# Kernel tuning notes

Hardware: AMD Instinct MI355X
Metric: run time of the kernel (lower is better)

The kernel has to match this reference:

```python
import jax, jax.numpy as jnp
import numpy as np

B, N, K, UP = 8, 2048, 20, 2
CIN, D, COUT, PH, AH = 256, 64, 128, 64, 256
EPS = 1e-5

def c1(x, W, b):
    # 1x1 Conv1d: x (B,C,N), W (O,C)
    return jnp.einsum('oc,bcn->bon', W, x) + b[None, :, None]

def c2(x, W, b):
    # 1x1 Conv2d: x (B,C,N,K), W (O,C)
    return jnp.einsum('oc,bcnk->bonk', W, x) + b[None, :, None, None]

def bn2(x, g, be):
    # eval-mode BatchNorm2d with running_mean=0, running_var=1
    inv = np.float32(1.0 / np.sqrt(1.0 + EPS))
    return g[None, :, None, None] * x * inv + be[None, :, None, None]

def knn_idx(p, k):
    # p: (B,N,3) -> (B,N,k) indices of k nearest neighbors (incl. self)
    sq = jnp.sum(p * p, -1)
    d = sq[:, :, None] + sq[:, None, :] - 2.0 * jnp.einsum('bnd,bmd->bnm', p, p)
    _, idx = jax.lax.top_k(-d, k)
    return idx

def group(feat, idx):
    # grouping_operation: feat (B,C,N), idx (B,N,k) -> (B,C,N,k)
    return jax.vmap(lambda f, i: f[:, i])(feat, idx)

def setup_inputs() -> dict:
    key = jax.random.key(0)
    ks = jax.random.split(key, 24)
    s = 0.02
    rn = lambda i, shp: jax.random.normal(ks[i], shp, jnp.float32) * s
    return {
        'pos': jax.random.normal(ks[0], (B, 3, N), jnp.float32),
        'key_feat': jax.random.normal(ks[1], (B, CIN, N), jnp.float32),
        'query_feat': jax.random.normal(ks[2], (B, CIN, N), jnp.float32),
        'upfeat': jax.random.normal(ks[3], (B, CIN, N), jnp.float32),
        # mlp_v (MLP_Res): in 2*CIN -> CIN -> CIN with shortcut
        'Wv1': rn(4, (CIN, 2 * CIN)), 'bv1': jnp.zeros(CIN, jnp.float32),
        'Wv2': rn(5, (CIN, CIN)), 'bv2': jnp.zeros(CIN, jnp.float32),
        'Wvs': rn(6, (CIN, 2 * CIN)), 'bvs': jnp.zeros(CIN, jnp.float32),
        # key/query/value/upfeat 1x1 convs CIN -> D
        'Wk': rn(7, (D, CIN)), 'bk': jnp.zeros(D, jnp.float32),
        'Wq': rn(8, (D, CIN)), 'bq': jnp.zeros(D, jnp.float32),
        'Wvv': rn(9, (D, CIN)), 'bvv': jnp.zeros(D, jnp.float32),
        'Wu': rn(10, (D, CIN)), 'bu': jnp.zeros(D, jnp.float32),
        # pos_mlp: 3 -> PH (BN, ReLU) -> D
        'Wp1': rn(11, (PH, 3)), 'bp1': jnp.zeros(PH, jnp.float32),
        'gp1': jnp.ones(PH, jnp.float32), 'betap1': jnp.zeros(PH, jnp.float32),
        'Wp2': rn(12, (D, PH)), 'bp2': jnp.zeros(D, jnp.float32),
        # attn_mlp: D -> AH (BN, ReLU) -> ConvTranspose2d(AH, D, (UP,1), (UP,1))
        'Wa1': rn(13, (AH, D)), 'ba1': jnp.zeros(AH, jnp.float32),
        'ga1': jnp.ones(AH, jnp.float32), 'betaa1': jnp.zeros(AH, jnp.float32),
        'Wt': rn(14, (AH, D, UP)), 'bt': jnp.zeros(D, jnp.float32),
        # conv_end D -> COUT, residual CIN -> COUT
        'Wend': rn(15, (COUT, D)), 'bend': jnp.zeros(COUT, jnp.float32),
        'Wres': rn(16, (COUT, CIN)), 'bres': jnp.zeros(COUT, jnp.float32),
    }

def reference(pos, key_feat, query_feat, upfeat,
              Wv1, bv1, Wv2, bv2, Wvs, bvs,
              Wk, bk, Wq, bq, Wvv, bvv, Wu, bu,
              Wp1, bp1, gp1, betap1, Wp2, bp2,
              Wa1, ba1, ga1, betaa1, Wt, bt,
              Wend, bend, Wres, bres):
    # mlp_v on concat(key, query)
    x = jnp.concatenate([key_feat, query_feat], axis=1)          # (B,2CIN,N)
    value = c1(jax.nn.relu(c1(x, Wv1, bv1)), Wv2, bv2) + c1(x, Wvs, bvs)
    identity = value                                             # (B,CIN,N)
    kf = c1(key_feat, Wk, bk)
    qf = c1(query_feat, Wq, bq)
    vf = c1(value, Wvv, bvv)                                     # (B,D,N)
    idx = knn_idx(pos.transpose(0, 2, 1), K)                     # (B,N,K)
    kg = group(kf, idx)                                          # (B,D,N,K)
    qk_rel = qf[:, :, :, None] - kg
    pos_rel = pos[:, :, :, None] - group(pos, idx)               # (B,3,N,K)
    pos_emb = c2(jax.nn.relu(bn2(c2(pos_rel, Wp1, bp1), gp1, betap1)), Wp2, bp2)
    uf = c1(upfeat, Wu, bu)
    u_rel = uf[:, :, :, None] - group(uf, idx)                   # (B,D,N,K)
    h = jax.nn.relu(bn2(c2(qk_rel + pos_emb + u_rel, Wa1, ba1), ga1, betaa1))  # (B,AH,N,K)
    b = h.shape[0]
    # ConvTranspose2d kernel (UP,1) stride (UP,1): expand N -> N*UP
    att = jnp.einsum('bhnk,hcr->bcnrk', h, Wt).reshape(b, D, N * UP, K) + bt[None, :, None, None]
    att = jax.nn.softmax(att, axis=-1)
    val = group(vf, idx) + pos_emb + u_rel                       # (B,D,N,K)
    val = jnp.repeat(val, UP, axis=2)                            # nearest Upsample (UP,1)
    agg = jnp.sum(att * val, axis=-1)                            # (B,D,N*UP)
    y = c1(agg, Wend, bend)                                      # (B,COUT,N*UP)
    ident = jnp.repeat(c1(identity, Wres, bres), UP, axis=2)     # residual path
    return y + ident
```

## Files before the change

kernel.cpp:

```cpp
#include <hip/hip_runtime.h>
#include <hip/hip_bf16.h>
#include <math.h>

#define BB 8
#define NN 2048
#define KK 20
#define UPF 2
#define CIN 256
#define DD 64
#define COUTN 128
#define PHH 64
#define AHH 256
#define BN_INV 0.9999950000374997f
#define NPB 8

typedef __hip_bfloat16 bf16;
typedef unsigned short u16;
typedef unsigned long long u64;
typedef _Float16 f16;
typedef _Float16 h2   __attribute__((ext_vector_type(2)));
typedef _Float16 f16x4 __attribute__((ext_vector_type(4)));
typedef _Float16 f16x8 __attribute__((ext_vector_type(8)));
typedef float    f32x4 __attribute__((ext_vector_type(4)));

static __device__ __forceinline__ float bf2f(const bf16 v) { return __bfloat162float(v); }
static __device__ __forceinline__ bf16  f2bf(const float v) { return __float2bfloat16(v); }
static __device__ __forceinline__ u16   f2bfu(const float v) {
    return __builtin_bit_cast(u16, __float2bfloat16(v));
}
static __device__ __forceinline__ float lo2f(const unsigned v) { return __builtin_bit_cast(float, v << 16); }
static __device__ __forceinline__ float hi2f(const unsigned v) { return __builtin_bit_cast(float, v & 0xFFFF0000u); }

static __device__ __forceinline__ f32x4 mfma16(const f16x8 a, const f16x8 b, const f32x4 c) {
    return __builtin_amdgcn_mfma_f32_16x16x32_f16(a, b, c, 0, 0, 0);
}
static __device__ __forceinline__ unsigned fmap(const float f) {
    unsigned u = __builtin_bit_cast(unsigned, f);
    return (u >> 31) ? ~u : (u | 0x80000000u);
}

__global__ void sentinel_kernel(float* out) {
    if (threadIdx.x == 0 && blockIdx.x == 0) out[0] = 100.0f;
}

__global__ __launch_bounds__(256) void prep_kernel(
    const float* __restrict__ Wa1, const float* __restrict__ Wp2,
    const float* __restrict__ Wend, const float* __restrict__ Wt,
    const float* __restrict__ Wv1, const float* __restrict__ Wv2,
    const float* __restrict__ Wvs, const float* __restrict__ Wvv,
    const float* __restrict__ Wres,
    const float* __restrict__ Wk, const float* __restrict__ Wq,
    const float* __restrict__ Wu,
    const float* __restrict__ ba1, const float* __restrict__ ga1,
    const float* __restrict__ betaa1,
    f16* __restrict__ Wa1h, f16* __restrict__ Wp2h, f16* __restrict__ Wth,
    float* __restrict__ A1s, float* __restrict__ A1b,
    f16* __restrict__ Wendh,
    f16* __restrict__ Wv1h, f16* __restrict__ Wv2h, f16* __restrict__ Wvsh,
    f16* __restrict__ Wvvh, f16* __restrict__ Wresh,
    f16* __restrict__ Wkh, f16* __restrict__ Wqh, f16* __restrict__ Wuh) {
    const int t = blockIdx.x * 256 + threadIdx.x;
    if (t < AHH * DD)        Wa1h[t] = (f16)Wa1[t];
    if (t < PHH * DD)        Wp2h[t] = (f16)Wp2[t];
    if (t < COUTN * AHH)     { int cr = t >> 8, hh = t & 255; Wth[t] = (f16)Wt[hh * COUTN + cr]; }
    if (t < AHH) {
        float gsc = ga1[t] * BN_INV;
        A1s[t] = gsc;
        A1b[t] = gsc * ba1[t] + betaa1[t];
    }
    if (t < COUTN * DD)      Wendh[t] = (f16)Wend[t];
    if (t < CIN * 2 * CIN)   Wv1h[t] = (f16)Wv1[t];
    if (t < CIN * CIN)       Wv2h[t] = (f16)Wv2[t];
    if (t < CIN * 2 * CIN)   Wvsh[t] = (f16)Wvs[t];
    if (t < DD * CIN)        Wvvh[t] = (f16)Wvv[t];
    if (t < COUTN * CIN)     Wresh[t] = (f16)Wres[t];
    if (t < DD * CIN)        Wkh[t]  = (f16)Wk[t];
    if (t < DD * CIN)        Wqh[t]  = (f16)Wq[t];
    if (t < DD * CIN)        Wuh[t]  = (f16)Wu[t];
}

__global__ __launch_bounds__(256) void xpose_kernel(
    const float* __restrict__ key_feat, const float* __restrict__ query_feat,
    const float* __restrict__ upfeat,
    f16* __restrict__ xkqT, f16* __restrict__ xuT) {
    __shared__ float tile[64][65];
    const int b  = blockIdx.x >> 5;
    const int n0 = (blockIdx.x & 31) << 6;
    const int y  = blockIdx.y;
    const int src = y >> 2;
    const int ct  = (y & 3) << 6;
    const int t = threadIdx.x;
    const float* xin = (src == 0) ? key_feat : (src == 1) ? query_feat : upfeat;
    f16* dst; int CT, cb;
    if (src < 2) { dst = xkqT; CT = 512; cb = src * 256 + ct; }
    else         { dst = xuT;  CT = 256; cb = ct; }
    for (int u = t; u < 64 * 64; u += 256) {
        const int c = u >> 6, j = u & 63;
        tile[c][j] = xin[((size_t)b * CIN + ct + c) * NN + n0 + j];
    }
    __syncthreads();
    for (int u = t; u < 64 * 32; u += 256) {
        const int n = u >> 5, c0 = (u & 31) << 1;
        h2 pr; pr.x = (f16)tile[c0][n]; pr.y = (f16)tile[c0 + 1][n];
        ((unsigned*)dst)[(((size_t)b * NN + n0 + n) * CT + cb + c0) >> 1] =
            __builtin_bit_cast(unsigned, pr);
    }
}

__global__ __launch_bounds__(256) void knn_kernel(const float* __restrict__ pos,
                                                  u16* __restrict__ idx_out,
                                                  float* __restrict__ posT) {
    __shared__ float dist[NN];
    __shared__ int   hist[512];
    __shared__ unsigned rmin[4], rmax[4];
    __shared__ u64   cbuf[64];
    __shared__ float q[3];
    __shared__ unsigned minkS;
    __shared__ int   shiftS, jstarS, cntS;
    __shared__ u64   ltbuf[KK];
    __shared__ int   tiebuf[64];
    __shared__ int   ri[4];
    __shared__ unsigned prefS;
    __shared__ int   knS, cnt_lt, cnt_eq;

    const int b = blockIdx.x / NN;
    const int n = blockIdx.x % NN;
    const int t = threadIdx.x;
    const float* pb = pos + (size_t)b * 3 * NN;
    const size_t rowKK = ((size_t)b * NN + n) * KK;

    if (t < 3) {
        float v = pb[(size_t)t * NN + n];
        q[t] = v;
        posT[((size_t)b * NN + n) * 3 + t] = v;
    }
    if (t == 0) { prefS = 0u; knS = KK; cnt_lt = 0; cnt_eq = 0; cntS = 0; jstarS = 0; }
    __syncthreads();
    const float qx = q[0], qy = q[1], qz = q[2];
    const float sqq = __fadd_rn(__fadd_rn(__fmul_rn(qx, qx), __fmul_rn(qy, qy)), __fmul_rn(qz, qz));
    unsigned kmin = 0xFFFFFFFFu, kmax = 0u;
    for (int m = t; m < NN; m += 256) {
        float px = pb[m];
        float py = pb[NN + m];
        float pz = pb[2 * NN + m];
        float sqm = __fadd_rn(__fadd_rn(__fmul_rn(px, px), __fmul_rn(py, py)), __fmul_rn(pz, pz));
        float dt  = __fadd_rn(__fadd_rn(__fmul_rn(qx, px), __fmul_rn(qy, py)), __fmul_rn(qz, pz));
        const float d = __fsub_rn(__fadd_rn(sqq, sqm), __fmul_rn(2.0f, dt));
        dist[m] = d;
        const unsigned key = fmap(d);
        kmin = min(kmin, key);
        kmax = max(kmax, key);
    }
#pragma unroll
    for (int off = 32; off > 0; off >>= 1) {
        kmin = min(kmin, (unsigned)__shfl_down((int)kmin, off, 64));
        kmax = max(kmax, (unsigned)__shfl_down((int)kmax, off, 64));
    }
    if ((t & 63) == 0) { rmin[t >> 6] = kmin; rmax[t >> 6] = kmax; }
    hist[t] = 0; hist[256 + t] = 0;
    __syncthreads();
    if (t == 0) {
        const unsigned mn = min(min(rmin[0], rmin[1]), min(rmin[2], rmin[3]));
        const unsigned mx = max(max(rmax[0], rmax[1]), max(rmax[2], rmax[3]));
        const unsigned range = mx - mn;
        minkS  = mn;
        shiftS = (range >= 256u) ? (24 - __clz((int)range)) : 0;
    }
    __syncthreads();
    const unsigned mink = minkS;
    const int sh = shiftS;

    for (int m = t; m < NN; m += 256) {
        const unsigned bin = (fmap(dist[m]) - mink) >> sh;
        atomicAdd(&hist[((unsigned)(t & 1) << 8) | bin], 1);
    }
    __syncthreads();
    if (t < 64) {
        const int h0  = hist[4 * t + 0] + hist[256 + 4 * t + 0];
        const int h1  = hist[4 * t + 1] + hist[256 + 4 * t + 1];
        const int h2v = hist[4 * t + 2] + hist[256 + 4 * t + 2];
        const int h3  = hist[4 * t + 3] + hist[256 + 4 * t + 3];
        const int lsum = h0 + h1 + h2v + h3;
        int incl = lsum;
#pragma unroll
        for (int off = 1; off < 64; off <<= 1) {
            int v = __shfl_up(incl, off, 64);
            if (t >= off) incl += v;
        }
        const int excl = incl - lsum;
        if (excl < KK && excl + lsum >= KK) {
            int bsel;
            if      (excl + h0 >= KK)            bsel = 0;
            else if (excl + h0 + h1 >= KK)       bsel = 1;
            else if (excl + h0 + h1 + h2v >= KK) bsel = 2;
            else                                 bsel = 3;
            jstarS = 4 * t + bsel;
        }
    }
    __syncthreads();
    const unsigned jstar = (unsigned)jstarS;

    for (int m = t; m < NN; m += 256) {
        const unsigned key = fmap(dist[m]);
        if (((key - mink) >> sh) <= jstar) {
            const int p = atomicAdd(&cntS, 1);
            if (p < 64) cbuf[p] = ((u64)key << 32) | (unsigned)m;
        }
    }
    __syncthreads();
    const int total = cntS;

    if (total <= 64) {
        if (t < 64) {
            u64 v = (t < total) ? cbuf[t] : 0xFFFFFFFFFFFFFFFFull;
            int rank = 0;
#pragma unroll 16
            for (int j = 0; j < 64; ++j) {
                const u64 o = (u64)__shfl((long long)v, j, 64);
                if (o < v) ++rank;
            }
            if (t < total && rank < KK) idx_out[rowKK + rank] = (u16)(v & 0xFFFFu);
        }
        return;
    }

    for (int pass = 0; pass < 4; ++pass) {
        const int shift = 24 - 8 * pass;
        const unsigned pm = (pass == 0) ? 0u : (0xFFFFFFFFu << (32 - 8 * pass));
        hist[t] = 0;
        __syncthreads();
        const unsigned pref = prefS;
        const int kn = knS;
        for (int m = t; m < NN; m += 256) {
            unsigned key = fmap(dist[m]);
            if ((key & pm) == pref)
                atomicAdd(&hist[(key >> shift) & 255], 1);
        }
        __syncthreads();
        if (t < 64) {
            const int h0 = hist[4 * t + 0], h1 = hist[4 * t + 1];
            const int h2v = hist[4 * t + 2], h3 = hist[4 * t + 3];
            const int lsum = h0 + h1 + h2v + h3;
            int incl = lsum;
#pragma unroll
            for (int off = 1; off < 64; off <<= 1) {
                int v = __shfl_up(incl, off, 64);
                if (t >= off) incl += v;
            }
            const int excl = incl - lsum;
            if (excl < kn && excl + lsum >= kn) {
                int bsel, cb;
                if      (excl + h0 >= kn)            { bsel = 0; cb = excl; }
                else if (excl + h0 + h1 >= kn)       { bsel = 1; cb = excl + h0; }
                else if (excl + h0 + h1 + h2v >= kn) { bsel = 2; cb = excl + h0 + h1; }
                else                                 { bsel = 3; cb = excl + h0 + h1 + h2v; }
                knS = kn - cb;
                prefS = pref | ((unsigned)(4 * t + bsel) << shift);
            }
        }
        __syncthreads();
    }

    const unsigned T = prefS;
    for (int m = t; m < NN; m += 256) {
        unsigned key = fmap(dist[m]);
        if (key < T) {
            int p = atomicAdd(&cnt_lt, 1);
            ltbuf[p] = ((u64)key << 32) | (unsigned)m;
        } else if (key == T) {
            int p = atomicAdd(&cnt_eq, 1);
            if (p < 64) tiebuf[p] = m;
        }
    }
    __syncthreads();
    const int nlt = cnt_lt, neq_need = knS, ceq = cnt_eq;

    if (t < 64) {
        u64 v = (t < nlt) ? ltbuf[t] : 0xFFFFFFFFFFFFFFFFull;
        int rank = 0;
#pragma unroll
        for (int j = 0; j < KK; ++j) {
            const u64 o = (u64)__shfl((long long)v, j, 64);
            if (o < v) ++rank;
        }
        if (t < nlt) idx_out[rowKK + rank] = (u16)(v & 0xFFFFu);
    }
    if (ceq <= 64) {
        if (t < 64) {
            int ti = (t < ceq) ? tiebuf[t] : 0x7FFFFFFF;
            int rk = 0;
            for (int j = 0; j < 64; ++j) {
                const int o = __shfl(ti, j, 64);
                if (o < ti) ++rk;
            }
            if (t < ceq && rk < neq_need) idx_out[rowKK + nlt + rk] = (u16)ti;
        }
    } else {
        for (int iter = 0; iter < neq_need; ++iter) {
            int bi = NN;
            for (int m = t; m < NN; m += 256)
                if (fmap(dist[m]) == T && m < bi) bi = m;
            for (int off = 32; off > 0; off >>= 1) {
                int i2 = __shfl_down(bi, off, 64);
                bi = min(bi, i2);
            }
            if ((t & 63) == 0) ri[t >> 6] = bi;
            __syncthreads();
            if (t == 0) {
                int i0 = min(min(ri[0], ri[1]), min(ri[2], ri[3]));
                idx_out[rowKK + nlt + iter] = (u16)i0;
                dist[i0] = 3.4e38f;
            }
            __syncthreads();
        }
    }
}

__global__ __launch_bounds__(256) void value_mfma(
    const f16* __restrict__ xkqT, const f16* __restrict__ xuT,
    const f16* __restrict__ Wv1h, const float* __restrict__ bv1,
    const f16* __restrict__ Wv2h, const float* __restrict__ bv2,
    const f16* __restrict__ Wvsh, const float* __restrict__ bvs,
    const f16* __restrict__ Wvvh, const float* __restrict__ bvv,
    const f16* __restrict__ Wresh, const float* __restrict__ bres,
    const f16* __restrict__ Wkh, const float* __restrict__ bk,
    const f16* __restrict__ Wqh, const float* __restrict__ bq,
    const f16* __restrict__ Wuh, const float* __restrict__ bu,
    bf16* __restrict__ vf_ws, bf16* __restrict__ resid_ws,
    bf16* __restrict__ kf, bf16* __restrict__ qf, bf16* __restrict__ uf) {
    __shared__ __align__(16) char hv[32 * 512];
    const int b  = blockIdx.x >> 6;
    const int n0 = (blockIdx.x & 63) << 5;
    const int t = threadIdx.x;
    const int w = t >> 6, l = t & 63, g = l >> 4, li = l & 15;
    const f16* xb = xkqT + ((size_t)b * NN + n0) * 512;
    const f32x4 zero4 = {0.f, 0.f, 0.f, 0.f};

    f32x4 a1[4][2];
    f32x4 ak[2] = {zero4, zero4}, aq[2] = {zero4, zero4};
#pragma unroll
    for (int mt = 0; mt < 4; ++mt) { a1[mt][0] = zero4; a1[mt][1] = zero4; }
    for (int ks = 0; ks < 16; ++ks) {
        f16x8 bx0 = *(const f16x8*)(xb + (size_t)li * 512 + ks * 32 + g * 8);
        f16x8 bx1 = *(const f16x8*)(xb + (size_t)(16 + li) * 512 + ks * 32 + g * 8);
#pragma unroll
        for (int mt = 0; mt < 4; ++mt) {
            const f16x8 af = *(const f16x8*)(Wv1h + (size_t)(w * 64 + mt * 16 + li) * 512 + ks * 32 + g * 8);
            a1[mt][0] = mfma16(af, bx0, a1[mt][0]);
            a1[mt][1] = mfma16(af, bx1, a1[mt][1]);
        }
        if (ks < 8) {
            const f16x8 afk = *(const f16x8*)(Wkh + (size_t)(w * 16 + li) * 256 + ks * 32 + g * 8);
            ak[0] = mfma16(afk, bx0, ak[0]);
            ak[1] = mfma16(afk, bx1, ak[1]);
        } else {
            const f16x8 afq = *(const f16x8*)(Wqh + (size_t)(w * 16 + li) * 256 + (ks - 8) * 32 + g * 8);
            aq[0] = mfma16(afq, bx0, aq[0]);
            aq[1] = mfma16(afq, bx1, aq[1]);
        }
    }
    f32x4 au[2] = {zero4, zero4};
    {
        const f16* xub = xuT + ((size_t)b * NN + n0) * 256;
        for (int ks = 0; ks < 8; ++ks) {
            f16x8 bu0 = *(const f16x8*)(xub + (size_t)li * 256 + ks * 32 + g * 8);
            f16x8 bu1 = *(const f16x8*)(xub + (size_t)(16 + li) * 256 + ks * 32 + g * 8);
            const f16x8 af = *(const f16x8*)(Wuh + (size_t)(w * 16 + li) * 256 + ks * 32 + g * 8);
            au[0] = mfma16(af, bu0, au[0]);
            au[1] = mfma16(af, bu1, au[1]);
        }
    }
#pragma unroll
    for (int mt = 0; mt < 4; ++mt) {
        const int ch0 = w * 64 + mt * 16 + g * 4;
        const float4 b4 = *(const float4*)(bv1 + ch0);
#pragma unroll
        for (int nt = 0; nt < 2; ++nt) {
            const int n = nt * 16 + li;
            f16x4 px;
            px.x = (f16)fmaxf(a1[mt][nt][0] + b4.x, 0.f);
            px.y = (f16)fmaxf(a1[mt][nt][1] + b4.y, 0.f);
            px.z = (f16)fmaxf(a1[mt][nt][2] + b4.z, 0.f);
            px.w = (f16)fmaxf(a1[mt][nt][3] + b4.w, 0.f);
            *(f16x4*)(hv + n * 512 + ((ch0 * 2) ^ ((n & 7) << 4))) = px;
        }
    }
    {
        const int ch0 = w * 16 + g * 4;
        const float4 bk4 = *(const float4*)(bk + ch0);
        const float4 bq4 = *(const float4*)(bq + ch0);
        const float4 bu4 = *(const float4*)(bu + ch0);
#pragma unroll
        for (int nt = 0; nt < 2; ++nt) {
            const int n = nt * 16 + li;
            const size_t base = ((size_t)b * NN + n0 + n) * DD + ch0;
            ushort4 pk, pq, pu;
            pk.x = f2bfu(ak[nt][0] + bk4.x); pk.y = f2bfu(ak[nt][1] + bk4.y);
            pk.z = f2bfu(ak[nt][2] + bk4.z); pk.w = f2bfu(ak[nt][3] + bk4.w);
            pq.x = f2bfu(aq[nt][0] + bq4.x); pq.y = f2bfu(aq[nt][1] + bq4.y);
            pq.z = f2bfu(aq[nt][2] + bq4.z); pq.w = f2bfu(aq[nt][3] + bq4.w);
            pu.x = f2bfu(au[nt][0] + bu4.x); pu.y = f2bfu(au[nt][1] + bu4.y);
            pu.z = f2bfu(au[nt][2] + bu4.z); pu.w = f2bfu(au[nt][3] + bu4.w);
            *(ushort4*)((char*)kf + base * 2) = pk;
            *(ushort4*)((char*)qf + base * 2) = pq;
            *(ushort4*)((char*)uf + base * 2) = pu;
        }
    }
    __syncthreads();

    f32x4 a2[4][2];
#pragma unroll
    for (int mt = 0; mt < 4; ++mt) { a2[mt][0] = zero4; a2[mt][1] = zero4; }
    for (int ks = 0; ks < 8; ++ks) {
        f16x8 bh[2];
#pragma unroll
        for (int nt = 0; nt < 2; ++nt) {
            const int n = nt * 16 + li;
            bh[nt] = *(const f16x8*)(hv + n * 512 + ((ks * 64 + g * 16) ^ ((n & 7) << 4)));
        }
#pragma unroll
        for (int mt = 0; mt < 4; ++mt) {
            const f16x8 af = *(const f16x8*)(Wv2h + (size_t)(w * 64 + mt * 16 + li) * 256 + ks * 32 + g * 8);
            a2[mt][0] = mfma16(af, bh[0], a2[mt][0]);
            a2[mt][1] = mfma16(af, bh[1], a2[mt][1]);
        }
    }
    for (int ks = 0; ks < 16; ++ks) {
        f16x8 bx0 = *(const f16x8*)(xb + (size_t)li * 512 + ks * 32 + g * 8);
        f16x8 bx1 = *(const f16x8*)(xb + (size_t)(16 + li) * 512 + ks * 32 + g * 8);
#pragma unroll
        for (int mt = 0; mt < 4; ++mt) {
            const f16x8 af = *(const f16x8*)(Wvsh + (size_t)(w * 64 + mt * 16 + li) * 512 + ks * 32 + g * 8);
            a2[mt][0] = mfma16(af, bx0, a2[mt][0]);
            a2[mt][1] = mfma16(af, bx1, a2[mt][1]);
        }
    }
    __syncthreads();
#pragma unroll
    for (int mt = 0; mt < 4; ++mt) {
        const int ch0 = w * 64 + mt * 16 + g * 4;
        const float4 c4a = *(const float4*)(bv2 + ch0);
        const float4 c4b = *(const float4*)(bvs + ch0);
#pragma unroll
        for (int nt = 0; nt < 2; ++nt) {
            const int n = nt * 16 + li;
            f16x4 px;
            px.x = (f16)(a2[mt][nt][0] + c4a.x + c4b.x);
            px.y = (f16)(a2[mt][nt][1] + c4a.y + c4b.y);
            px.z = (f16)(a2[mt][nt][2] + c4a.z + c4b.z);
            px.w = (f16)(a2[mt][nt][3] + c4a.w + c4b.w);
            *(f16x4*)(hv + n * 512 + ((ch0 * 2) ^ ((n & 7) << 4))) = px;
        }
    }
    __syncthreads();

    f32x4 av[2] = {zero4, zero4};
    f32x4 ar[2][2];
    ar[0][0] = zero4; ar[0][1] = zero4; ar[1][0] = zero4; ar[1][1] = zero4;
    for (int ks = 0; ks < 8; ++ks) {
        f16x8 bh[2];
#pragma unroll
        for (int nt = 0; nt < 2; ++nt) {
            const int n = nt * 16 + li;
            bh[nt] = *(const f16x8*)(hv + n * 512 + ((ks * 64 + g * 16) ^ ((n & 7) << 4)));
        }
        const f16x8 afv = *(const f16x8*)(Wvvh + (size_t)(w * 16 + li) * 256 + ks * 32 + g * 8);
        av[0] = mfma16(afv, bh[0], av[0]);
        av[1] = mfma16(afv, bh[1], av[1]);
#pragma unroll
        for (int rt = 0; rt < 2; ++rt) {
            const f16x8 afr = *(const f16x8*)(Wresh + (size_t)((w * 2 + rt) * 16 + li) * 256 + ks * 32 + g * 8);
            ar[rt][0] = mfma16(afr, bh[0], ar[rt][0]);
            ar[rt][1] = mfma16(afr, bh[1], ar[rt][1]);
        }
    }
    {
        const int ch0 = w * 16 + g * 4;
        const float4 bb = *(const float4*)(bvv + ch0);
#pragma unroll
        for (int nt = 0; nt < 2; ++nt) {
            const int n = nt * 16 + li;
            ushort4 pk;
            pk.x = f2bfu(av[nt][0] + bb.x);
            pk.y = f2bfu(av[nt][1] + bb.y);
            pk.z = f2bfu(av[nt][2] + bb.z);
            pk.w = f2bfu(av[nt][3] + bb.w);
            *(ushort4*)((char*)vf_ws + (((size_t)b * NN + n0 + n) * DD + ch0) * 2) = pk;
        }
    }
#pragma unroll
    for (int rt = 0; rt < 2; ++rt) {
        const int ch0 = (w * 2 + rt) * 16 + g * 4;
        const float4 bb = *(const float4*)(bres + ch0);
#pragma unroll
        for (int nt = 0; nt < 2; ++nt) {
            const int n = nt * 16 + li;
            ushort4 pk;
            pk.x = f2bfu(ar[rt][nt][0] + bb.x);
            pk.y = f2bfu(ar[rt][nt][1] + bb.y);
            pk.z = f2bfu(ar[rt][nt][2] + bb.z);
            pk.w = f2bfu(ar[rt][nt][3] + bb.w);
            *(ushort4*)((char*)resid_ws + (((size_t)b * NN + n0 + n) * COUTN + ch0) * 2) = pk;
        }
    }
}

__global__ __launch_bounds__(512, 4) void attn_fused(
    const float* __restrict__ posT, const u16* __restrict__ idx_ws,
    const bf16* __restrict__ kf_ws, const bf16* __restrict__ qf_ws,
    const bf16* __restrict__ uf_ws, const bf16* __restrict__ vf_ws,
    const bf16* __restrict__ resid_ws,
    const float* __restrict__ Wp1, const float* __restrict__ bp1,
    const float* __restrict__ gp1, const float* __restrict__ betap1,
    const f16* __restrict__ Wp2h, const float* __restrict__ bp2,
    const f16* __restrict__ Wa1h, const float* __restrict__ A1s,
    const float* __restrict__ A1b, const f16* __restrict__ Wth,
    const f16* __restrict__ Wendh, const float* __restrict__ bend,
    float* __restrict__ out) {
    __shared__ __align__(16) char pool[61440];
    f16*  ph16 = (f16*)(pool);
    f16*  S16  = (f16*)(pool);
    f16*  L16T = (f16*)(pool);
    f16*  peh  = (f16*)(pool + 20480);
    char* Hl   = pool + 20480;
    f16*  V16  = (f16*)(pool + 40960);
    __shared__ __align__(16) f16 aggf[16 * 64];
    __shared__ int   nidx[8 * KK];
    __shared__ float prel[8 * KK][3];
    __shared__ float qcol[NPB][64], ucol[NPB][64];

    const int b  = blockIdx.x >> 8;
    const int n0 = (blockIdx.x & 255) << 3;
    const int t = threadIdx.x;
    const int w = t >> 6, l = t & 63, g = l >> 4, li = l & 15;
    const int m4 = w & 3, nh = w >> 2;
    const size_t row0 = (size_t)b * NN + n0;
    const f32x4 zero4 = {0.f, 0.f, 0.f, 0.f};

    if (t < 8 * KK) nidx[t] = (int)idx_ws[row0 * KK + t];
    __syncthreads();

    {
        const int n = t >> 6, c = t & 63;
        qcol[n][c] = bf2f(qf_ws[(row0 + n) * DD + c]);
        ucol[n][c] = bf2f(uf_ws[(row0 + n) * DD + c]);
    }
    if (t < 480) {
        const int r = t / 3, d = t - r * 3;
        const int n = r / KK;
        prel[r][d] = posT[(row0 + n) * 3 + d] - posT[((size_t)b * NN + nidx[r]) * 3 + d];
    }
    __syncthreads();

    for (int u = t; u < 160 * 32; u += 512) {
        const int r = u >> 5, c0 = (u & 31) << 1;
        float a0 = Wp1[c0 * 3 + 0] * prel[r][0] + Wp1[c0 * 3 + 1] * prel[r][1]
                 + Wp1[c0 * 3 + 2] * prel[r][2] + bp1[c0];
        float a1 = Wp1[c0 * 3 + 3] * prel[r][0] + Wp1[c0 * 3 + 4] * prel[r][1]
                 + Wp1[c0 * 3 + 5] * prel[r][2] + bp1[c0 + 1];
        a0 = gp1[c0] * a0 * BN_INV + betap1[c0];
        a1 = gp1[c0 + 1] * a1 * BN_INV + betap1[c0 + 1];
        h2 pr; pr.x = (f16)fmaxf(a0, 0.f); pr.y = (f16)fmaxf(a1, 0.f);
        *(unsigned*)((char*)ph16 + (r * 128 + ((c0 * 2) ^ ((r & 7) << 4)))) =
            __builtin_bit_cast(unsigned, pr);
    }
    __syncthreads();

    {
        f32x4 d[5];
#pragma unroll
        for (int j = 0; j < 5; ++j) d[j] = zero4;
#pragma unroll
        for (int ks = 0; ks < 2; ++ks) {
            const f16x8 af = *(const f16x8*)(Wp2h + (m4 * 16 + li) * 64 + ks * 32 + g * 8);
#pragma unroll
            for (int j = 0; j < 5; ++j) {
                const int r = (nh * 5 + j) * 16 + li;
                const f16x8 bf = *(const f16x8*)((const char*)ph16 +
                                  (r * 128 + ((ks * 64 + g * 16) ^ ((r & 7) << 4))));
                d[j] = mfma16(af, bf, d[j]);
            }
        }
        const int ch0 = m4 * 16 + g * 4;
        const float4 b4 = *(const float4*)(bp2 + ch0);
#pragma unroll
        for (int j = 0; j < 5; ++j) {
            const int r = (nh * 5 + j) * 16 + li;
            f16x4 pk;
            pk.x = (f16)(d[j][0] + b4.x);
            pk.y = (f16)(d[j][1] + b4.y);
            pk.z = (f16)(d[j][2] + b4.z);
            pk.w = (f16)(d[j][3] + b4.w);
            *(f16x4*)((char*)peh + (r * 128 + ((ch0 * 2) ^ ((r & 7) << 4)))) = pk;
        }
    }
    __syncthreads();

    for (int u = t; u < 160 * 32; u += 512) {
        const int r = u >> 5, c0 = (u & 31) << 1;
        const int n = r / KK;
        const size_t nb2 = (((size_t)b * NN + nidx[r]) * DD + c0) * 2;
        const unsigned kq = *(const unsigned*)((const char*)kf_ws + nb2);
        const unsigned uq = *(const unsigned*)((const char*)uf_ws + nb2);
        const unsigned vq = *(const unsigned*)((const char*)vf_ws + nb2);
        const unsigned pw = *(const unsigned*)((const char*)peh +
                              (r * 128 + ((c0 * 2) ^ ((r & 7) << 4))));
        const h2 pp = __builtin_bit_cast(h2, pw);
        const float add0 = ucol[n][c0] + (float)pp.x;
        const float add1 = ucol[n][c0 + 1] + (float)pp.y;
        const float gb0 = -(lo2f(kq) + lo2f(uq));
        const float gb1 = -(hi2f(kq) + hi2f(uq));
        const float vb0 = lo2f(vq) - lo2f(uq);
        const float vb1 = hi2f(vq) - hi2f(uq);
        h2 s; s.x = (f16)(gb0 + qcol[n][c0] + add0); s.y = (f16)(gb1 + qcol[n][c0 + 1] + add1);
        h2 v; v.x = (f16)(vb0 + add0);               v.y = (f16)(vb1 + add1);
        const int sw = (c0 * 2) ^ ((r & 7) << 4);
        *(unsigned*)((char*)S16 + (r * 128 + sw)) = __builtin_bit_cast(unsigned, s);
        *(unsigned*)((char*)V16 + (r * 128 + sw)) = __builtin_bit_cast(unsigned, v);
    }
    __syncthreads();

    f32x4 acc2[10];
#pragma unroll
    for (int j = 0; j < 10; ++j) acc2[j] = zero4;

    for (int c4 = 0; c4 < 4; ++c4) {
        const int hrb = c4 * 64 + m4 * 16;
        f32x4 d1[5];
#pragma unroll
        for (int j = 0; j < 5; ++j) d1[j] = zero4;
#pragma unroll
        for (int ks = 0; ks < 2; ++ks) {
            const f16x8 af = *(const f16x8*)(Wa1h + (hrb + li) * 64 + ks * 32 + g * 8);
#pragma unroll
            for (int j = 0; j < 5; ++j) {
                const int r = (nh * 5 + j) * 16 + li;
                const f16x8 sfv = *(const f16x8*)((const char*)S16 +
                                   (r * 128 + ((ks * 64 + g * 16) ^ ((r & 7) << 4))));
                d1[j] = mfma16(af, sfv, d1[j]);
            }
        }
        const float4 as4 = *(const float4*)(A1s + hrb + g * 4);
        const float4 ab4 = *(const float4*)(A1b + hrb + g * 4);
        __syncthreads();
#pragma unroll
        for (int j = 0; j < 5; ++j) {
            const int col = (nh * 5 + j) * 16 + li;
            const int ch0 = m4 * 16 + g * 4;
            f16x4 pk;
            pk.x = (f16)fmaxf(as4.x * d1[j][0] + ab4.x, 0.f);
            pk.y = (f16)fmaxf(as4.y * d1[j][1] + ab4.y, 0.f);
            pk.z = (f16)fmaxf(as4.z * d1[j][2] + ab4.z, 0.f);
            pk.w = (f16)fmaxf(as4.w * d1[j][3] + ab4.w, 0.f);
            *(f16x4*)(Hl + col * 128 + ((ch0 * 2) ^ ((col & 7) << 4))) = pk;
        }
        __syncthreads();
#pragma unroll
        for (int ks2 = 0; ks2 < 2; ++ks2) {
            const f16x8 bf = *(const f16x8*)(Wth + (size_t)(w * 16 + li) * AHH + c4 * 64 + ks2 * 32 + g * 8);
#pragma unroll
            for (int nt = 0; nt < 10; ++nt) {
                const int col = nt * 16 + li;
                const f16x8 ha = *(const f16x8*)(Hl + col * 128 + ((ks2 * 64 + g * 16) ^ ((col & 7) << 4)));
                acc2[nt] = mfma16(ha, bf, acc2[nt]);
            }
        }
    }
    __syncthreads();

#pragma unroll
    for (int nt = 0; nt < 10; ++nt) {
        const f32x4 d = acc2[nt];
#pragma unroll
        for (int j = 0; j < 4; ++j) {
            const int row = nt * 16 + g * 4 + j;
            *(f16*)((char*)L16T + (row * 256 + (((w * 16 + li) * 2) ^ ((row & 3) << 5)))) =
                (f16)d[j];
        }
    }
    __syncthreads();

    {
        const int cr = t & 127, c = cr >> 1, rr = cr & 1;
        const int nbase = (t >> 7) * 2;
        for (int p = 0; p < 2; ++p) {
            const int n = nbase + p;
            float lv[20];
#pragma unroll
            for (int k = 0; k < 20; ++k) {
                const int row = n * KK + k;
                lv[k] = (float)*(const f16*)((const char*)L16T +
                          (row * 256 + ((cr * 2) ^ ((row & 3) << 5))));
            }
            float m = lv[0];
#pragma unroll
            for (int k = 1; k < 20; ++k) m = fmaxf(m, lv[k]);
            float s = 0.f, a = 0.f;
#pragma unroll
            for (int k = 0; k < 20; ++k) {
                const float e = __expf(lv[k] - m);
                s += e;
                const int r = n * KK + k;
                const float vv = (float)*(const f16*)((const char*)V16 +
                                   (r * 128 + ((c * 2) ^ ((r & 7) << 4))));
                a += e * vv;
            }
            const int arow = n * 2 + rr;
            *(f16*)((char*)aggf + (arow * 128 + ((c * 2) ^ ((arow & 7) << 4)))) = (f16)(a / s);
        }
    }
    __syncthreads();

    {
        f32x4 dc = zero4;
#pragma unroll
        for (int ks = 0; ks < 2; ++ks) {
            const f16x8 af = *(const f16x8*)(Wendh + (size_t)(w * 16 + li) * 64 + ks * 32 + g * 8);
            const f16x8 bfr = *(const f16x8*)((const char*)aggf +
                               (li * 128 + (((ks * 32 + g * 8) * 2) ^ ((li & 7) << 4))));
            dc = mfma16(af, bfr, dc);
        }
        const int nloc = li >> 1;
#pragma unroll
        for (int j = 0; j < 4; ++j) {
            const int o = w * 16 + g * 4 + j;
            const float rv = bf2f(resid_ws[(row0 + nloc) * COUTN + o]);
            out[(size_t)b * COUTN * (NN * UPF) + (size_t)o * (NN * UPF) + 2 * n0 + li] =
                dc[j] + bend[o] + rv;
        }
    }
}

extern "C" void kernel_launch(void* const* d_in, const int* in_sizes, int n_in,
                              void* d_out, int out_size, void* d_ws, size_t ws_size,
                              hipStream_t stream) {
    const float* pos        = (const float*)d_in[0];
    const float* key_feat   = (const float*)d_in[1];
    const float* query_feat = (const float*)d_in[2];
    const float* upfeat     = (const float*)d_in[3];
    const float* Wv1 = (const float*)d_in[4];
    const float* bv1 = (const float*)d_in[5];
    const float* Wv2 = (const float*)d_in[6];
    const float* bv2 = (const float*)d_in[7];
    const float* Wvs = (const float*)d_in[8];
    const float* bvs = (const float*)d_in[9];
    const float* Wk  = (const float*)d_in[10];
    const float* bk  = (const float*)d_in[11];
    const float* Wq  = (const float*)d_in[12];
    const float* bq  = (const float*)d_in[13];
    const float* Wvv = (const float*)d_in[14];
    const float* bvv = (const float*)d_in[15];
    const float* Wu  = (const float*)d_in[16];
    const float* bu  = (const float*)d_in[17];
    const float* Wp1 = (const float*)d_in[18];
    const float* bp1 = (const float*)d_in[19];
    const float* gp1 = (const float*)d_in[20];
    const float* betap1 = (const float*)d_in[21];
    const float* Wp2 = (const float*)d_in[22];
    const float* bp2 = (const float*)d_in[23];
    const float* Wa1 = (const float*)d_in[24];
    const float* ba1 = (const float*)d_in[25];
    const float* ga1 = (const float*)d_in[26];
    const float* betaa1 = (const float*)d_in[27];
    const float* Wt   = (const float*)d_in[28];
    const float* bt   = (const float*)d_in[29];
    const float* Wend = (const float*)d_in[30];
    const float* bend = (const float*)d_in[31];
    const float* Wres = (const float*)d_in[32];
    const float* bres = (const float*)d_in[33];
    float* out = (float*)d_out;
    (void)out_size; (void)bt;

    const bool sizes_ok = (n_in >= 34)
        && (in_sizes[0] == BB * 3 * NN)
        && (in_sizes[1] == BB * CIN * NN)
        && (in_sizes[4] == CIN * 2 * CIN)
        && (in_sizes[28] == AHH * DD * UPF)
        && (in_sizes[32] == COUTN * CIN);

    size_t off = 0;
    auto take = [&](size_t bytes) { size_t o = off; off = (off + bytes + 255) & ~(size_t)255; return o; };
    const size_t off_posT  = take((size_t)BB * NN * 3 * sizeof(float));
    const size_t off_idx   = take((size_t)BB * NN * KK * sizeof(u16));
    const size_t off_vf    = take((size_t)BB * NN * DD * sizeof(bf16));
    const size_t off_kf    = take((size_t)BB * NN * DD * sizeof(bf16));
    const size_t off_qf    = take((size_t)BB * NN * DD * sizeof(bf16));
    const size_t off_uf    = take((size_t)BB * NN * DD * sizeof(bf16));
    const size_t off_resid = take((size_t)BB * NN * COUTN * sizeof(bf16));
    const size_t off_wa1h  = take((size_t)AHH * DD * sizeof(f16));
    const size_t off_wp2h  = take((size_t)PHH * DD * sizeof(f16));
    const size_t off_wth   = take((size_t)COUTN * AHH * sizeof(f16));
    const size_t off_a1s   = take((size_t)AHH * sizeof(float));
    const size_t off_a1b   = take((size_t)AHH * sizeof(float));
    const size_t off_wendh = take((size_t)COUTN * DD * sizeof(f16));
    const size_t off_wv1h  = take((size_t)CIN * 2 * CIN * sizeof(f16));
    const size_t off_wv2h  = take((size_t)CIN * CIN * sizeof(f16));
    const size_t off_wvsh  = take((size_t)CIN * 2 * CIN * sizeof(f16));
    const size_t off_wvvh  = take((size_t)DD * CIN * sizeof(f16));
    const size_t off_wresh = take((size_t)COUTN * CIN * sizeof(f16));
    const size_t off_wkh   = take((size_t)DD * CIN * sizeof(f16));
    const size_t off_wqh   = take((size_t)DD * CIN * sizeof(f16));
    const size_t off_wuh   = take((size_t)DD * CIN * sizeof(f16));
    const size_t off_xkq   = take((size_t)BB * NN * 512 * sizeof(f16));
    const size_t off_xu    = take((size_t)BB * NN * 256 * sizeof(f16));
    const size_t NEED = off;

    if (!sizes_ok) return;
    if (ws_size < NEED) {
        sentinel_kernel<<<1, 64, 0, stream>>>(out);
        return;
    }

    char* ws = (char*)d_ws;
    float* posT_ws  = (float*)(ws + off_posT);
    u16*   idx_ws   = (u16*)(ws + off_idx);
    bf16*  vf_ws    = (bf16*)(ws + off_vf);
    bf16*  kf_ws    = (bf16*)(ws + off_kf);
    bf16*  qf_ws    = (bf16*)(ws + off_qf);
    bf16*  uf_ws    = (bf16*)(ws + off_uf);
    bf16*  resid_ws = (bf16*)(ws + off_resid);
    f16*   Wa1h_ws  = (f16*)(ws + off_wa1h);
    f16*   Wp2h_ws  = (f16*)(ws + off_wp2h);
    f16*   Wth_ws   = (f16*)(ws + off_wth);
    float* A1s_ws   = (float*)(ws + off_a1s);
    float* A1b_ws   = (float*)(ws + off_a1b);
    f16*   Wendh_ws = (f16*)(ws + off_wendh);
    f16*   Wv1h_ws  = (f16*)(ws + off_wv1h);
    f16*   Wv2h_ws  = (f16*)(ws + off_wv2h);
    f16*   Wvsh_ws  = (f16*)(ws + off_wvsh);
    f16*   Wvvh_ws  = (f16*)(ws + off_wvvh);
    f16*   Wresh_ws = (f16*)(ws + off_wresh);
    f16*   Wkh_ws   = (f16*)(ws + off_wkh);
    f16*   Wqh_ws   = (f16*)(ws + off_wqh);
    f16*   Wuh_ws   = (f16*)(ws + off_wuh);
    f16*   xkqT_ws  = (f16*)(ws + off_xkq);
    f16*   xuT_ws   = (f16*)(ws + off_xu);

    prep_kernel<<<(CIN * 2 * CIN + 255) / 256, 256, 0, stream>>>(
        Wa1, Wp2, Wend, Wt, Wv1, Wv2, Wvs, Wvv, Wres, Wk, Wq, Wu,
        ba1, ga1, betaa1,
        Wa1h_ws, Wp2h_ws, Wth_ws, A1s_ws, A1b_ws, Wendh_ws,
        Wv1h_ws, Wv2h_ws, Wvsh_ws, Wvvh_ws, Wresh_ws, Wkh_ws, Wqh_ws, Wuh_ws);
    xpose_kernel<<<dim3(BB * (NN / 64), 12), 256, 0, stream>>>(
        key_feat, query_feat, upfeat, xkqT_ws, xuT_ws);
    knn_kernel<<<BB * NN, 256, 0, stream>>>(pos, idx_ws, posT_ws);
    value_mfma<<<BB * (NN / 32), 256, 0, stream>>>(xkqT_ws, xuT_ws,
        Wv1h_ws, bv1, Wv2h_ws, bv2, Wvsh_ws, bvs, Wvvh_ws, bvv, Wresh_ws, bres,
        Wkh_ws, bk, Wqh_ws, bq, Wuh_ws, bu,
        vf_ws, resid_ws, kf_ws, qf_ws, uf_ws);
    attn_fused<<<BB * (NN / NPB), 512, 0, stream>>>(posT_ws, idx_ws,
        kf_ws, qf_ws, uf_ws, vf_ws, resid_ws,
        Wp1, bp1, gp1, betap1, Wp2h_ws, bp2,
        Wa1h_ws, A1s_ws, A1b_ws, Wth_ws, Wendh_ws, bend, out);
}
```

Before: 426.7 us.

## Double points per attention block to 16 with 1024 threads and vectorized gathers

The fused attention kernel now handles 16 points per block using 1024 threads, with shared memory doubled to about 120KB. Work is redistributed so each wave takes an output-channel quarter and half of the neighbor rows in the transpose-conv and final conv MFMA stages. The goal is to reuse the per-block weight fragment loads (Wth, Wend) across more points and cut block count. The neighbor gather loop also moves from 4-byte to 16-byte loads. The cost is lower occupancy, since launch bounds now allow one 1024-thread block and large LDS use. Some sub-stages may also run with a partial mapping.

```diff
diff --git a/kernel.cpp b/kernel.cpp
--- a/kernel.cpp
+++ b/kernel.cpp
@@ -12,7 +12,7 @@
 #define PHH 64
 #define AHH 256
 #define BN_INV 0.9999950000374997f
-#define NPB 8
+#define NPB 16
 
 typedef __hip_bfloat16 bf16;
 typedef unsigned short u16;
@@ -505,7 +505,7 @@
     }
 }
 
-__global__ __launch_bounds__(512, 4) void attn_fused(
+__global__ __launch_bounds__(1024, 1) void attn_fused(
     const float* __restrict__ posT, const u16* __restrict__ idx_ws,
     const bf16* __restrict__ kf_ws, const bf16* __restrict__ qf_ws,
     const bf16* __restrict__ uf_ws, const bf16* __restrict__ vf_ws,
@@ -517,27 +517,28 @@
     const float* __restrict__ A1b, const f16* __restrict__ Wth,
     const f16* __restrict__ Wendh, const float* __restrict__ bend,
     float* __restrict__ out) {
-    __shared__ __align__(16) char pool[61440];
+    __shared__ __align__(16) char pool[122880];
     f16*  ph16 = (f16*)(pool);
     f16*  S16  = (f16*)(pool);
     f16*  L16T = (f16*)(pool);
-    f16*  peh  = (f16*)(pool + 20480);
-    char* Hl   = pool + 20480;
-    f16*  V16  = (f16*)(pool + 40960);
-    __shared__ __align__(16) f16 aggf[16 * 64];
-    __shared__ int   nidx[8 * KK];
-    __shared__ float prel[8 * KK][3];
+    f16*  peh  = (f16*)(pool + 40960);
+    char* Hl   = pool + 40960;
+    f16*  V16  = (f16*)(pool + 81920);
+    __shared__ __align__(16) f16 aggf[32 * 64];
+    __shared__ int   nidx[NPB * KK];
+    __shared__ float prel[NPB * KK][3];
     __shared__ float qcol[NPB][64], ucol[NPB][64];
 
-    const int b  = blockIdx.x >> 8;
-    const int n0 = (blockIdx.x & 255) << 3;
+    const int b  = blockIdx.x >> 7;
+    const int n0 = (blockIdx.x & 127) << 4;
     const int t = threadIdx.x;
     const int w = t >> 6, l = t & 63, g = l >> 4, li = l & 15;
-    const int m4 = w & 3, nh = w >> 2;
+    const int m4 = w & 3, nh = (w >> 2) & 3;
+    const int cq = w & 7, nhf = w >> 3;
     const size_t row0 = (size_t)b * NN + n0;
     const f32x4 zero4 = {0.f, 0.f, 0.f, 0.f};
 
-    if (t < 8 * KK) nidx[t] = (int)idx_ws[row0 * KK + t];
+    if (t < NPB * KK) nidx[t] = (int)idx_ws[row0 * KK + t];
     __syncthreads();
 
     {
@@ -545,14 +546,14 @@
         qcol[n][c] = bf2f(qf_ws[(row0 + n) * DD + c]);
         ucol[n][c] = bf2f(uf_ws[(row0 + n) * DD + c]);
     }
-    if (t < 480) {
+    if (t < 960) {
         const int r = t / 3, d = t - r * 3;
         const int n = r / KK;
         prel[r][d] = posT[(row0 + n) * 3 + d] - posT[((size_t)b * NN + nidx[r]) * 3 + d];
     }
     __syncthreads();
 
-    for (int u = t; u < 160 * 32; u += 512) {
+    for (int u = t; u < 320 * 32; u += 1024) {
         const int r = u >> 5, c0 = (u & 31) << 1;
         float a0 = Wp1[c0 * 3 + 0] * prel[r][0] + Wp1[c0 * 3 + 1] * prel[r][1]
                  + Wp1[c0 * 3 + 2] * prel[r][2] + bp1[c0];
@@ -596,27 +597,32 @@
     }
     __syncthreads();
 
-    for (int u = t; u < 160 * 32; u += 512) {
-        const int r = u >> 5, c0 = (u & 31) << 1;
+    for (int u = t; u < 320 * 8; u += 1024) {
+        const int r = u >> 3, cg = (u & 7) << 3;
         const int n = r / KK;
-        const size_t nb2 = (((size_t)b * NN + nidx[r]) * DD + c0) * 2;
-        const unsigned kq = *(const unsigned*)((const char*)kf_ws + nb2);
-        const unsigned uq = *(const unsigned*)((const char*)uf_ws + nb2);
-        const unsigned vq = *(const unsigned*)((const char*)vf_ws + nb2);
-        const unsigned pw = *(const unsigned*)((const char*)peh +
-                              (r * 128 + ((c0 * 2) ^ ((r & 7) << 4))));
-        const h2 pp = __builtin_bit_cast(h2, pw);
-        const float add0 = ucol[n][c0] + (float)pp.x;
-        const float add1 = ucol[n][c0 + 1] + (float)pp.y;
-        const float gb0 = -(lo2f(kq) + lo2f(uq));
-        const float gb1 = -(hi2f(kq) + hi2f(uq));
-        const float vb0 = lo2f(vq) - lo2f(uq);
-        const float vb1 = hi2f(vq) - hi2f(uq);
-        h2 s; s.x = (f16)(gb0 + qcol[n][c0] + add0); s.y = (f16)(gb1 + qcol[n][c0 + 1] + add1);
-        h2 v; v.x = (f16)(vb0 + add0);               v.y = (f16)(vb1 + add1);
-        const int sw = (c0 * 2) ^ ((r & 7) << 4);
-        *(unsigned*)((char*)S16 + (r * 128 + sw)) = __builtin_bit_cast(unsigned, s);
-        *(unsigned*)((char*)V16 + (r * 128 + sw)) = __builtin_bit_cast(unsigned, v);
+        const size_t nb = (((size_t)b * NN + nidx[r]) * DD + cg) * 2;
+        const uint4 kq = *(const uint4*)((const char*)kf_ws + nb);
+        const uint4 uq = *(const uint4*)((const char*)uf_ws + nb);
+        const uint4 vq = *(const uint4*)((const char*)vf_ws + nb);
+        const int sw = (cg * 2) ^ ((r & 7) << 4);
+        const uint4 pw = *(const uint4*)((const char*)peh + (r * 128 + sw));
+        uint4 sres, vres;
+#define PROC(comp, off) { \
+        const float k0 = lo2f(kq.comp), k1 = hi2f(kq.comp); \
+        const float u0 = lo2f(uq.comp), u1 = hi2f(uq.comp); \
+        const float v0 = lo2f(vq.comp), v1 = hi2f(vq.comp); \
+        const h2 pp = __builtin_bit_cast(h2, pw.comp); \
+        const float add0 = ucol[n][cg + off]     + (float)pp.x; \
+        const float add1 = ucol[n][cg + off + 1] + (float)pp.y; \
+        h2 s; s.x = (f16)(-(k0 + u0) + qcol[n][cg + off] + add0); \
+              s.y = (f16)(-(k1 + u1) + qcol[n][cg + off + 1] + add1); \
+        h2 v; v.x = (f16)(v0 - u0 + add0); v.y = (f16)(v1 - u1 + add1); \
+        sres.comp = __builtin_bit_cast(unsigned, s); \
+        vres.comp = __builtin_bit_cast(unsigned, v); }
+        PROC(x, 0) PROC(y, 2) PROC(z, 4) PROC(w, 6)
+#undef PROC
+        *(uint4*)((char*)S16 + (r * 128 + sw)) = sres;
+        *(uint4*)((char*)V16 + (r * 128 + sw)) = vres;
     }
     __syncthreads();
 
@@ -657,25 +663,25 @@
         __syncthreads();
 #pragma unroll
         for (int ks2 = 0; ks2 < 2; ++ks2) {
-            const f16x8 bf = *(const f16x8*)(Wth + (size_t)(w * 16 + li) * AHH + c4 * 64 + ks2 * 32 + g * 8);
-#pragma unroll
-            for (int nt = 0; nt < 10; ++nt) {
-                const int col = nt * 16 + li;
+            const f16x8 bf = *(const f16x8*)(Wth + (size_t)(cq * 16 + li) * AHH + c4 * 64 + ks2 * 32 + g * 8);
+#pragma unroll
+            for (int j = 0; j < 10; ++j) {
+                const int col = (nhf * 10 + j) * 16 + li;
                 const f16x8 ha = *(const f16x8*)(Hl + col * 128 + ((ks2 * 64 + g * 16) ^ ((col & 7) << 4)));
-                acc2[nt] = mfma16(ha, bf, acc2[nt]);
-            }
-        }
-    }
-    __syncthreads();
-
-#pragma unroll
-    for (int nt = 0; nt < 10; ++nt) {
-        const f32x4 d = acc2[nt];
-#pragma unroll
-        for (int j = 0; j < 4; ++j) {
-            const int row = nt * 16 + g * 4 + j;
-            *(f16*)((char*)L16T + (row * 256 + (((w * 16 + li) * 2) ^ ((row & 3) << 5)))) =
-                (f16)d[j];
+                acc2[j] = mfma16(ha, bf, acc2[j]);
+            }
+        }
+    }
+    __syncthreads();
+
+#pragma unroll
+    for (int j = 0; j < 10; ++j) {
+        const f32x4 d = acc2[j];
+#pragma unroll
+        for (int jj = 0; jj < 4; ++jj) {
+            const int row = (nhf * 10 + j) * 16 + g * 4 + jj;
+            *(f16*)((char*)L16T + (row * 256 + (((cq * 16 + li) * 2) ^ ((row & 3) << 5)))) =
+                (f16)d[jj];
         }
     }
     __syncthreads();
@@ -712,20 +718,22 @@
     __syncthreads();
 
     {
+        const int ot = w & 7, ntile = w >> 3;
+        const int nr = ntile * 16 + li;
         f32x4 dc = zero4;
 #pragma unroll
         for (int ks = 0; ks < 2; ++ks) {
-            const f16x8 af = *(const f16x8*)(Wendh + (size_t)(w * 16 + li) * 64 + ks * 32 + g * 8);
+            const f16x8 af = *(const f16x8*)(Wendh + (size_t)(ot * 16 + li) * 64 + ks * 32 + g * 8);
             const f16x8 bfr = *(const f16x8*)((const char*)aggf +
-                               (li * 128 + (((ks * 32 + g * 8) * 2) ^ ((li & 7) << 4))));
+                               (nr * 128 + (((ks * 32 + g * 8) * 2) ^ ((nr & 7) << 4))));
             dc = mfma16(af, bfr, dc);
         }
-        const int nloc = li >> 1;
+        const int nloc = nr >> 1;
 #pragma unroll
         for (int j = 0; j < 4; ++j) {
-            const int o = w * 16 + g * 4 + j;
+            const int o = ot * 16 + g * 4 + j;
             const float rv = bf2f(resid_ws[(row0 + nloc) * COUTN + o]);
-            out[(size_t)b * COUTN * (NN * UPF) + (size_t)o * (NN * UPF) + 2 * n0 + li] =
+            out[(size_t)b * COUTN * (NN * UPF) + (size_t)o * (NN * UPF) + 2 * n0 + nr] =
                 dc[j] + bend[o] + rv;
         }
     }
@@ -848,7 +856,7 @@
         Wv1h_ws, bv1, Wv2h_ws, bv2, Wvsh_ws, bvs, Wvvh_ws, bvv, Wresh_ws, bres,
         Wkh_ws, bk, Wqh_ws, bq, Wuh_ws, bu,
         vf_ws, resid_ws, kf_ws, qf_ws, uf_ws);
-    attn_fused<<<BB * (NN / NPB), 512, 0, stream>>>(posT_ws, idx_ws,
+    attn_fused<<<BB * (NN / NPB), 1024, 0, stream>>>(posT_ws, idx_ws,
         kf_ws, qf_ws, uf_ws, vf_ws, resid_ws,
         Wp1, bp1, gp1, betap1, Wp2h_ws, bp2,
         Wa1h_ws, A1s_ws, A1b_ws, Wth_ws, Wendh_ws, bend, out);
```

Result: slower. 435.8 us (+2.1%).
